# Performance work log

Hardware: AMD Instinct MI355X
Metric: run time of the kernel (lower is better)

## Reference

```python
import jax, jax.numpy as jnp
import numpy as np

RES = 8          # voxel_resolution
CLASSES = 40
B, N = 64, 100000


def setup_inputs() -> dict:
    key = jax.random.key(0)
    kx, kw, kb = jax.random.split(key, 3)
    x = jax.random.normal(kx, (B, N, 3), dtype=jnp.float32)
    f = RES ** 3
    # nn.Linear(f, CLASSES): W is (out, in), uniform(-1/sqrt(in), 1/sqrt(in))
    bound = 1.0 / np.sqrt(f)
    W = jax.random.uniform(kw, (CLASSES, f), dtype=jnp.float32, minval=-bound, maxval=bound)
    b = jax.random.uniform(kb, (CLASSES,), dtype=jnp.float32, minval=-bound, maxval=bound)
    return {"x": x, "W": W, "b": b}


def _count_points(x):
    # x: (B, N, 3) -> per-batch adaptive-range 3D histogram, normalized by N
    b_, n_, _ = x.shape
    mins = x.min(axis=1, keepdims=True)            # (B,1,3)
    maxs = x.max(axis=1, keepdims=True)            # (B,1,3)
    rng = maxs - mins
    scale = RES / jnp.where(rng > 0, rng, 1.0)
    # bin index per point per dim; points at max fall in last bin (histogramdd
    # right-closes the final bin) -> clip to RES-1
    idx = jnp.clip(jnp.floor((x - mins) * scale).astype(jnp.int32), 0, RES - 1)  # (B,N,3)
    flat = (idx[..., 0] * RES + idx[..., 1]) * RES + idx[..., 2]                 # (B,N)
    flat = flat + (jnp.arange(b_, dtype=jnp.int32) * (RES ** 3))[:, None]
    counts = jax.ops.segment_sum(
        jnp.ones((b_ * n_,), dtype=x.dtype),
        flat.reshape(-1),
        num_segments=b_ * RES ** 3,
    ).reshape(b_, RES ** 3)
    return counts / n_


def reference(x, W, b):
    counts = _count_points(x)           # (B, RES^3), mode='count'
    logits = counts @ W.T + b           # (B, CLASSES)
    return logits
```

## Files before the change

### kernel.cpp

```cpp
#include <hip/hip_runtime.h>
#include <hip/hip_cooperative_groups.h>

namespace cg = cooperative_groups;

#define RES 8
#define F 512
#define CLASSES 40
#define B 64
#define NPTS 100000
#define NSLOT (NPTS / 4)

#define BLKS 16

#define PARTH_OFF 0
#define PARTMM_OFF (B * BLKS * F)

__global__ __launch_bounds__(256, 4) void fused_kernel(const float* __restrict__ x,
                                                       const float* __restrict__ Wm,
                                                       const float* __restrict__ bias,
                                                       float* __restrict__ out,
                                                       unsigned int* __restrict__ ws) {
    const int sub   = blockIdx.x;
    const int batch = blockIdx.y;
    const int t     = threadIdx.x;

    __shared__ unsigned int lh[4][F];
    __shared__ float red[6][BLKS];
    __shared__ float smn[3], ssc[3];
    __shared__ float wmin[4][3], wmax[4][3];
    __shared__ float cf[F];

    for (int i = t; i < 4 * F; i += 256) ((unsigned int*)lh)[i] = 0u;

    const float4* xb4 = (const float4*)(x + (size_t)batch * (NPTS * 3));

    {
        float m0 = 3.0e38f, m1 = 3.0e38f, m2 = 3.0e38f;
        float M0 = -3.0e38f, M1 = -3.0e38f, M2 = -3.0e38f;
        for (int i = sub * 256 + t; i < NSLOT; i += BLKS * 256) {
            float4 p0 = xb4[3 * i + 0];
            float4 p1 = xb4[3 * i + 1];
            float4 p2 = xb4[3 * i + 2];
            m0 = fminf(m0, fminf(fminf(p0.x, p0.w), fminf(p1.z, p2.y)));
            M0 = fmaxf(M0, fmaxf(fmaxf(p0.x, p0.w), fmaxf(p1.z, p2.y)));
            m1 = fminf(m1, fminf(fminf(p0.y, p1.x), fminf(p1.w, p2.z)));
            M1 = fmaxf(M1, fmaxf(fmaxf(p0.y, p1.x), fmaxf(p1.w, p2.z)));
            m2 = fminf(m2, fminf(fminf(p0.z, p1.y), fminf(p2.x, p2.w)));
            M2 = fmaxf(M2, fmaxf(fmaxf(p0.z, p1.y), fmaxf(p2.x, p2.w)));
        }
        for (int d = 1; d < 64; d <<= 1) {
            m0 = fminf(m0, __shfl_xor(m0, d)); M0 = fmaxf(M0, __shfl_xor(M0, d));
            m1 = fminf(m1, __shfl_xor(m1, d)); M1 = fmaxf(M1, __shfl_xor(M1, d));
            m2 = fminf(m2, __shfl_xor(m2, d)); M2 = fmaxf(M2, __shfl_xor(M2, d));
        }
        const int wave = t >> 6;
        if ((t & 63) == 0) {
            wmin[wave][0] = m0; wmin[wave][1] = m1; wmin[wave][2] = m2;
            wmax[wave][0] = M0; wmax[wave][1] = M1; wmax[wave][2] = M2;
        }
        __syncthreads();
        if (t < 3) {
            float mn = fminf(fminf(wmin[0][t], wmin[1][t]), fminf(wmin[2][t], wmin[3][t]));
            float mx = fmaxf(fmaxf(wmax[0][t], wmax[1][t]), fmaxf(wmax[2][t], wmax[3][t]));
            float* pm = (float*)(ws + PARTMM_OFF) + ((size_t)batch * BLKS + sub) * 6;
            pm[t]     = mn;
            pm[3 + t] = mx;
        }
    }

    cg::this_grid().sync();

    {
        const float* pm = (const float*)(ws + PARTMM_OFF) + (size_t)batch * BLKS * 6;
        if (t < 6 * BLKS) {
            const int c = t % 6, j = t / 6;
            red[c][j] = pm[j * 6 + c];
        }
        __syncthreads();
        if (t < 3) {
            float mn = red[t][0], mx = red[t + 3][0];
#pragma unroll
            for (int j = 1; j < BLKS; ++j) {
                mn = fminf(mn, red[t][j]);
                mx = fmaxf(mx, red[t + 3][j]);
            }
            float rng = mx - mn;
            smn[t] = mn;
            ssc[t] = (float)RES / (rng > 0.0f ? rng : 1.0f);
        }
        __syncthreads();
    }

    {
        const float mn0 = smn[0], mn1 = smn[1], mn2 = smn[2];
        const float sc0 = ssc[0], sc1 = ssc[1], sc2 = ssc[2];
        unsigned int* myh = lh[t >> 6];

        for (int i = sub * 256 + t; i < NSLOT; i += BLKS * 256) {
            float4 p0 = xb4[3 * i + 0];
            float4 p1 = xb4[3 * i + 1];
            float4 p2 = xb4[3 * i + 2];
            float px[4][3] = {{p0.x, p0.y, p0.z},
                              {p0.w, p1.x, p1.y},
                              {p1.z, p1.w, p2.x},
                              {p2.y, p2.z, p2.w}};
#pragma unroll
            for (int q = 0; q < 4; ++q) {
                int i0 = (int)floorf((px[q][0] - mn0) * sc0);
                int i1 = (int)floorf((px[q][1] - mn1) * sc1);
                int i2 = (int)floorf((px[q][2] - mn2) * sc2);
                i0 = min(max(i0, 0), RES - 1);
                i1 = min(max(i1, 0), RES - 1);
                i2 = min(max(i2, 0), RES - 1);
                atomicAdd(&myh[(i0 * RES + i1) * RES + i2], 1u);
            }
        }
        __syncthreads();

        unsigned int* ph = ws + PARTH_OFF + ((size_t)batch * BLKS + sub) * F;
        for (int bin = t; bin < F; bin += 256)
            ph[bin] = lh[0][bin] + lh[1][bin] + lh[2][bin] + lh[3][bin];
    }

    cg::this_grid().sync();

    if (sub != 0) return;
    {
        const unsigned int* ph = ws + PARTH_OFF + (size_t)batch * BLKS * F;
        for (int bin = t; bin < F; bin += 256) {
            unsigned int s = 0;
#pragma unroll
            for (int j = 0; j < BLKS; ++j) s += ph[j * F + bin];
            cf[bin] = (float)s * (1.0f / (float)NPTS);
        }
        __syncthreads();
        if (t < CLASSES) {
            const float4* wr  = (const float4*)(Wm + t * F);
            const float4* cf4 = (const float4*)cf;
            float d0 = 0.f, d1 = 0.f, d2 = 0.f, d3 = 0.f;
#pragma unroll 4
            for (int k = 0; k < F / 4; k += 4) {
                float4 w0 = wr[k],   c0 = cf4[k];
                float4 w1 = wr[k+1], c1 = cf4[k+1];
                float4 w2 = wr[k+2], c2 = cf4[k+2];
                float4 w3 = wr[k+3], c3 = cf4[k+3];
                d0 += c0.x*w0.x + c0.y*w0.y + c0.z*w0.z + c0.w*w0.w;
                d1 += c1.x*w1.x + c1.y*w1.y + c1.z*w1.z + c1.w*w1.w;
                d2 += c2.x*w2.x + c2.y*w2.y + c2.z*w2.z + c2.w*w2.w;
                d3 += c3.x*w3.x + c3.y*w3.y + c3.z*w3.z + c3.w*w3.w;
            }
            out[batch * CLASSES + t] = ((d0 + d1) + (d2 + d3)) + bias[t];
        }
    }
}

__global__ __launch_bounds__(256) void minmax_kernel(const float* __restrict__ x,
                                                     unsigned int* __restrict__ ws) {
    const int sub = blockIdx.x, batch = blockIdx.y, t = threadIdx.x;
    const float4* xb4 = (const float4*)(x + (size_t)batch * (NPTS * 3));
    float m0 = 3.0e38f, m1 = 3.0e38f, m2 = 3.0e38f;
    float M0 = -3.0e38f, M1 = -3.0e38f, M2 = -3.0e38f;
    for (int i = sub * 256 + t; i < NSLOT; i += BLKS * 256) {
        float4 p0 = xb4[3 * i + 0];
        float4 p1 = xb4[3 * i + 1];
        float4 p2 = xb4[3 * i + 2];
        m0 = fminf(m0, fminf(fminf(p0.x, p0.w), fminf(p1.z, p2.y)));
        M0 = fmaxf(M0, fmaxf(fmaxf(p0.x, p0.w), fmaxf(p1.z, p2.y)));
        m1 = fminf(m1, fminf(fminf(p0.y, p1.x), fminf(p1.w, p2.z)));
        M1 = fmaxf(M1, fmaxf(fmaxf(p0.y, p1.x), fmaxf(p1.w, p2.z)));
        m2 = fminf(m2, fminf(fminf(p0.z, p1.y), fminf(p2.x, p2.w)));
        M2 = fmaxf(M2, fmaxf(fmaxf(p0.z, p1.y), fmaxf(p2.x, p2.w)));
    }
    for (int d = 1; d < 64; d <<= 1) {
        m0 = fminf(m0, __shfl_xor(m0, d)); M0 = fmaxf(M0, __shfl_xor(M0, d));
        m1 = fminf(m1, __shfl_xor(m1, d)); M1 = fmaxf(M1, __shfl_xor(M1, d));
        m2 = fminf(m2, __shfl_xor(m2, d)); M2 = fmaxf(M2, __shfl_xor(M2, d));
    }
    __shared__ float wmin[4][3], wmax[4][3];
    const int wave = t >> 6;
    if ((t & 63) == 0) {
        wmin[wave][0] = m0; wmin[wave][1] = m1; wmin[wave][2] = m2;
        wmax[wave][0] = M0; wmax[wave][1] = M1; wmax[wave][2] = M2;
    }
    __syncthreads();
    if (t < 3) {
        float mn = fminf(fminf(wmin[0][t], wmin[1][t]), fminf(wmin[2][t], wmin[3][t]));
        float mx = fmaxf(fmaxf(wmax[0][t], wmax[1][t]), fmaxf(wmax[2][t], wmax[3][t]));
        float* pm = (float*)(ws + PARTMM_OFF) + ((size_t)batch * BLKS + sub) * 6;
        pm[t] = mn;
        pm[3 + t] = mx;
    }
}

__global__ __launch_bounds__(256) void hist_kernel(const float* __restrict__ x,
                                                   unsigned int* __restrict__ ws) {
    const int sub = blockIdx.x, batch = blockIdx.y, t = threadIdx.x;
    __shared__ unsigned int lh[4][F];
    __shared__ float red[6][BLKS];
    __shared__ float smn[3], ssc[3];
    for (int i = t; i < 4 * F; i += 256) ((unsigned int*)lh)[i] = 0u;

    const float* pm = (const float*)(ws + PARTMM_OFF) + (size_t)batch * BLKS * 6;
    if (t < 6 * BLKS) {
        const int c = t % 6, j = t / 6;
        red[c][j] = pm[j * 6 + c];
    }
    __syncthreads();
    if (t < 3) {
        float mn = red[t][0], mx = red[t + 3][0];
#pragma unroll
        for (int j = 1; j < BLKS; ++j) {
            mn = fminf(mn, red[t][j]);
            mx = fmaxf(mx, red[t + 3][j]);
        }
        float rng = mx - mn;
        smn[t] = mn;
        ssc[t] = (float)RES / (rng > 0.0f ? rng : 1.0f);
    }
    __syncthreads();

    const float mn0 = smn[0], mn1 = smn[1], mn2 = smn[2];
    const float sc0 = ssc[0], sc1 = ssc[1], sc2 = ssc[2];
    const float4* xb4 = (const float4*)(x + (size_t)batch * (NPTS * 3));
    unsigned int* myh = lh[t >> 6];
    for (int i = sub * 256 + t; i < NSLOT; i += BLKS * 256) {
        float4 p0 = xb4[3 * i + 0];
        float4 p1 = xb4[3 * i + 1];
        float4 p2 = xb4[3 * i + 2];
        float px[4][3] = {{p0.x, p0.y, p0.z},
                          {p0.w, p1.x, p1.y},
                          {p1.z, p1.w, p2.x},
                          {p2.y, p2.z, p2.w}};
#pragma unroll
        for (int q = 0; q < 4; ++q) {
            int i0 = (int)floorf((px[q][0] - mn0) * sc0);
            int i1 = (int)floorf((px[q][1] - mn1) * sc1);
            int i2 = (int)floorf((px[q][2] - mn2) * sc2);
            i0 = min(max(i0, 0), RES - 1);
            i1 = min(max(i1, 0), RES - 1);
            i2 = min(max(i2, 0), RES - 1);
            atomicAdd(&myh[(i0 * RES + i1) * RES + i2], 1u);
        }
    }
    __syncthreads();
    unsigned int* ph = ws + PARTH_OFF + ((size_t)batch * BLKS + sub) * F;
    for (int bin = t; bin < F; bin += 256)
        ph[bin] = lh[0][bin] + lh[1][bin] + lh[2][bin] + lh[3][bin];
}

__global__ __launch_bounds__(256) void logits_kernel(const unsigned int* __restrict__ ws,
                                                     const float* __restrict__ Wm,
                                                     const float* __restrict__ bias,
                                                     float* __restrict__ out) {
    const int batch = blockIdx.x, t = threadIdx.x;
    __shared__ float cf[F];
    const unsigned int* ph = ws + PARTH_OFF + (size_t)batch * BLKS * F;
    for (int bin = t; bin < F; bin += 256) {
        unsigned int s = 0;
#pragma unroll
        for (int j = 0; j < BLKS; ++j) s += ph[j * F + bin];
        cf[bin] = (float)s * (1.0f / (float)NPTS);
    }
    __syncthreads();
    if (t < CLASSES) {
        const float4* wr  = (const float4*)(Wm + t * F);
        const float4* cf4 = (const float4*)cf;
        float d0 = 0.f, d1 = 0.f, d2 = 0.f, d3 = 0.f;
#pragma unroll 4
        for (int k = 0; k < F / 4; k += 4) {
            float4 w0 = wr[k],   c0 = cf4[k];
            float4 w1 = wr[k+1], c1 = cf4[k+1];
            float4 w2 = wr[k+2], c2 = cf4[k+2];
            float4 w3 = wr[k+3], c3 = cf4[k+3];
            d0 += c0.x*w0.x + c0.y*w0.y + c0.z*w0.z + c0.w*w0.w;
            d1 += c1.x*w1.x + c1.y*w1.y + c1.z*w1.z + c1.w*w1.w;
            d2 += c2.x*w2.x + c2.y*w2.y + c2.z*w2.z + c2.w*w2.w;
            d3 += c3.x*w3.x + c3.y*w3.y + c3.z*w3.z + c3.w*w3.w;
        }
        out[batch * CLASSES + t] = ((d0 + d1) + (d2 + d3)) + bias[t];
    }
}

extern "C" void kernel_launch(void* const* d_in, const int* in_sizes, int n_in,
                              void* d_out, int out_size, void* d_ws, size_t ws_size,
                              hipStream_t stream) {
    const float* x    = (const float*)d_in[0];
    const float* Wm   = (const float*)d_in[1];
    const float* bias = (const float*)d_in[2];
    float* out        = (float*)d_out;
    unsigned int* ws  = (unsigned int*)d_ws;

    static int coop_ok = -1;
    if (coop_ok < 0) {
        int dev = 0;
        hipGetDevice(&dev);
        hipDeviceProp_t prop{};
        hipGetDeviceProperties(&prop, dev);
        int nb = 0;
        hipError_t e = hipOccupancyMaxActiveBlocksPerMultiprocessor(
            &nb, (const void*)fused_kernel, 256, 0);
        coop_ok = (e == hipSuccess && prop.cooperativeLaunch &&
                   (long)nb * prop.multiProcessorCount >= (long)BLKS * B) ? 1 : 0;
    }

    if (coop_ok) {
        void* args[] = {(void*)&x, (void*)&Wm, (void*)&bias, (void*)&out, (void*)&ws};
        hipLaunchCooperativeKernel((const void*)fused_kernel, dim3(BLKS, B), dim3(256),
                                   args, 0, stream);
    } else {
        minmax_kernel<<<dim3(BLKS, B), 256, 0, stream>>>(x, ws);
        hist_kernel<<<dim3(BLKS, B), 256, 0, stream>>>(x, ws);
        logits_kernel<<<B, 256, 0, stream>>>(ws, Wm, bias, out);
    }
}
```

Baseline: 126.8 us.

## Replace grid-wide cooperative syncs with per-batch flag spin-waits

Drops the two cooperative-groups grid barriers and replaces them with per-batch release/acquire flags, padded to separate slots, that each block polls with s_sleep. Batches can then advance independently instead of waiting for all 1024 blocks. Block 0 of each batch now reuses its own shared-memory histogram instead of writing it out and reading it back, and the min/max scan loop is unrolled by two. The flags use a fixed magic value. If the workspace is not cleared between launches, stale flags from an earlier call could satisfy the waits, and spinning also assumes all blocks of a batch are co-resident.

```diff
diff --git a/kernel.cpp b/kernel.cpp
--- a/kernel.cpp
+++ b/kernel.cpp
@@ -1,7 +1,4 @@
 #include <hip/hip_runtime.h>
-#include <hip/hip_cooperative_groups.h>
-
-namespace cg = cooperative_groups;
 
 #define RES 8
 #define F 512
@@ -12,8 +9,12 @@
 
 #define BLKS 16
 
+#define MAGIC 0x5F3A9C71u
+
 #define PARTH_OFF 0
 #define PARTMM_OFF (B * BLKS * F)
+#define FLAGMM_OFF (PARTMM_OFF + B * BLKS * 6)
+#define FLAGH_OFF  (FLAGMM_OFF + B * BLKS * 16)
 
 __global__ __launch_bounds__(256, 4) void fused_kernel(const float* __restrict__ x,
                                                        const float* __restrict__ Wm,
@@ -37,6 +38,7 @@
     {
         float m0 = 3.0e38f, m1 = 3.0e38f, m2 = 3.0e38f;
         float M0 = -3.0e38f, M1 = -3.0e38f, M2 = -3.0e38f;
+#pragma unroll 2
         for (int i = sub * 256 + t; i < NSLOT; i += BLKS * 256) {
             float4 p0 = xb4[3 * i + 0];
             float4 p1 = xb4[3 * i + 1];
@@ -68,7 +70,19 @@
         }
     }
 
-    cg::this_grid().sync();
+    __syncthreads();
+    if (t == 0) {
+        __threadfence();
+        __hip_atomic_store(&ws[FLAGMM_OFF + (batch * BLKS + sub) * 16], MAGIC,
+                           __ATOMIC_RELEASE, __HIP_MEMORY_SCOPE_AGENT);
+    }
+    if (t < BLKS) {
+        const unsigned int* fl = &ws[FLAGMM_OFF + (batch * BLKS + t) * 16];
+        while (__hip_atomic_load(fl, __ATOMIC_ACQUIRE, __HIP_MEMORY_SCOPE_AGENT) != MAGIC)
+            __builtin_amdgcn_s_sleep(2);
+    }
+    __syncthreads();
+    __threadfence();
 
     {
         const float* pm = (const float*)(ws + PARTMM_OFF) + (size_t)batch * BLKS * 6;
@@ -116,21 +130,34 @@
             }
         }
         __syncthreads();
-
+    }
+
+    if (sub != 0) {
         unsigned int* ph = ws + PARTH_OFF + ((size_t)batch * BLKS + sub) * F;
         for (int bin = t; bin < F; bin += 256)
             ph[bin] = lh[0][bin] + lh[1][bin] + lh[2][bin] + lh[3][bin];
-    }
-
-    cg::this_grid().sync();
-
-    if (sub != 0) return;
+        __syncthreads();
+        if (t == 0) {
+            __threadfence();
+            __hip_atomic_store(&ws[FLAGH_OFF + (batch * BLKS + sub) * 16], MAGIC,
+                               __ATOMIC_RELEASE, __HIP_MEMORY_SCOPE_AGENT);
+        }
+        return;
+    }
+
+    if (t >= 1 && t < BLKS) {
+        const unsigned int* fl = &ws[FLAGH_OFF + (batch * BLKS + t) * 16];
+        while (__hip_atomic_load(fl, __ATOMIC_ACQUIRE, __HIP_MEMORY_SCOPE_AGENT) != MAGIC)
+            __builtin_amdgcn_s_sleep(2);
+    }
+    __syncthreads();
+    __threadfence();
     {
         const unsigned int* ph = ws + PARTH_OFF + (size_t)batch * BLKS * F;
         for (int bin = t; bin < F; bin += 256) {
-            unsigned int s = 0;
-#pragma unroll
-            for (int j = 0; j < BLKS; ++j) s += ph[j * F + bin];
+            unsigned int s = lh[0][bin] + lh[1][bin] + lh[2][bin] + lh[3][bin];
+#pragma unroll
+            for (int j = 1; j < BLKS; ++j) s += ph[j * F + bin];
             cf[bin] = (float)s * (1.0f / (float)NPTS);
         }
         __syncthreads();
```

After: 130.7 us. 3.1% more time.

## Hold point data in registers across passes; replace final grid sync with counter

Applied to the files above, without the earlier changes.

Each thread in the fused kernel now loads its six (plus an optional tail) 48-byte point groups once into registers. It reuses them for both the min/max reduction and the histogram binning, so the input is no longer read from global memory twice. The trailing cooperative grid sync before the logits stage is replaced with a per-batch atomic counter, and the last block to finish a batch computes that batch's logits. The register-resident loads raise VGPR pressure, and the counter scheme depends on correct fences and on the counter reset ordering relative to the earlier cross-block sync.

```diff
diff --git a/kernel.cpp b/kernel.cpp
--- a/kernel.cpp
+++ b/kernel.cpp
@@ -11,9 +11,39 @@
 #define NSLOT (NPTS / 4)
 
 #define BLKS 16
+#define TPB (BLKS * 256)
+#define NFULL 6
+#define TAILCUT (NSLOT - NFULL * TPB)
 
 #define PARTH_OFF 0
 #define PARTMM_OFF (B * BLKS * F)
+#define CNT_OFF (PARTMM_OFF + B * BLKS * 6)
+
+#define MM4(pA, pB, pC) do { \
+    m0 = fminf(m0, fminf(fminf((pA).x, (pA).w), fminf((pB).z, (pC).y))); \
+    M0 = fmaxf(M0, fmaxf(fmaxf((pA).x, (pA).w), fmaxf((pB).z, (pC).y))); \
+    m1 = fminf(m1, fminf(fminf((pA).y, (pB).x), fminf((pB).w, (pC).z))); \
+    M1 = fmaxf(M1, fmaxf(fmaxf((pA).y, (pB).x), fmaxf((pB).w, (pC).z))); \
+    m2 = fminf(m2, fminf(fminf((pA).z, (pB).y), fminf((pC).x, (pC).w))); \
+    M2 = fmaxf(M2, fmaxf(fmaxf((pA).z, (pB).y), fmaxf((pC).x, (pC).w))); \
+} while (0)
+
+#define BIN1(X, Y, Z) do { \
+    int i0 = (int)floorf(((X) - mn0) * sc0); \
+    int i1 = (int)floorf(((Y) - mn1) * sc1); \
+    int i2 = (int)floorf(((Z) - mn2) * sc2); \
+    i0 = min(max(i0, 0), RES - 1); \
+    i1 = min(max(i1, 0), RES - 1); \
+    i2 = min(max(i2, 0), RES - 1); \
+    atomicAdd(&myh[(i0 * RES + i1) * RES + i2], 1u); \
+} while (0)
+
+#define BIN4(pA, pB, pC) do { \
+    BIN1((pA).x, (pA).y, (pA).z); \
+    BIN1((pA).w, (pB).x, (pB).y); \
+    BIN1((pB).z, (pB).w, (pC).x); \
+    BIN1((pC).y, (pC).z, (pC).w); \
+} while (0)
 
 __global__ __launch_bounds__(256, 4) void fused_kernel(const float* __restrict__ x,
                                                        const float* __restrict__ Wm,
@@ -29,24 +59,38 @@
     __shared__ float smn[3], ssc[3];
     __shared__ float wmin[4][3], wmax[4][3];
     __shared__ float cf[F];
+    __shared__ int swin;
 
     for (int i = t; i < 4 * F; i += 256) ((unsigned int*)lh)[i] = 0u;
 
+    if (sub == 0 && t == 0)
+        __hip_atomic_store(&ws[CNT_OFF + batch * 16], 0u,
+                           __ATOMIC_RELAXED, __HIP_MEMORY_SCOPE_AGENT);
+
     const float4* xb4 = (const float4*)(x + (size_t)batch * (NPTS * 3));
+    const int g = sub * 256 + t;
+    const float4* bp = xb4 + 3 * g;
+    const bool tail = (g < TAILCUT);
+
+    float4 c0a = bp[0],         c0b = bp[1],         c0c = bp[2];
+    float4 c1a = bp[12288],     c1b = bp[12289],     c1c = bp[12290];
+    float4 c2a = bp[24576],     c2b = bp[24577],     c2c = bp[24578];
+    float4 c3a = bp[36864],     c3b = bp[36865],     c3c = bp[36866];
+    float4 c4a = bp[49152],     c4b = bp[49153],     c4c = bp[49154];
+    float4 c5a = bp[61440],     c5b = bp[61441],     c5c = bp[61442];
 
     {
         float m0 = 3.0e38f, m1 = 3.0e38f, m2 = 3.0e38f;
         float M0 = -3.0e38f, M1 = -3.0e38f, M2 = -3.0e38f;
-        for (int i = sub * 256 + t; i < NSLOT; i += BLKS * 256) {
-            float4 p0 = xb4[3 * i + 0];
-            float4 p1 = xb4[3 * i + 1];
-            float4 p2 = xb4[3 * i + 2];
-            m0 = fminf(m0, fminf(fminf(p0.x, p0.w), fminf(p1.z, p2.y)));
-            M0 = fmaxf(M0, fmaxf(fmaxf(p0.x, p0.w), fmaxf(p1.z, p2.y)));
-            m1 = fminf(m1, fminf(fminf(p0.y, p1.x), fminf(p1.w, p2.z)));
-            M1 = fmaxf(M1, fmaxf(fmaxf(p0.y, p1.x), fmaxf(p1.w, p2.z)));
-            m2 = fminf(m2, fminf(fminf(p0.z, p1.y), fminf(p2.x, p2.w)));
-            M2 = fmaxf(M2, fmaxf(fmaxf(p0.z, p1.y), fmaxf(p2.x, p2.w)));
+        MM4(c0a, c0b, c0c);
+        MM4(c1a, c1b, c1c);
+        MM4(c2a, c2b, c2c);
+        MM4(c3a, c3b, c3c);
+        MM4(c4a, c4b, c4c);
+        MM4(c5a, c5b, c5c);
+        if (tail) {
+            float4 ta = bp[73728], tb = bp[73729], tc = bp[73730];
+            MM4(ta, tb, tc);
         }
         for (int d = 1; d < 64; d <<= 1) {
             m0 = fminf(m0, __shfl_xor(m0, d)); M0 = fmaxf(M0, __shfl_xor(M0, d));
@@ -96,35 +140,35 @@
         const float sc0 = ssc[0], sc1 = ssc[1], sc2 = ssc[2];
         unsigned int* myh = lh[t >> 6];
 
-        for (int i = sub * 256 + t; i < NSLOT; i += BLKS * 256) {
-            float4 p0 = xb4[3 * i + 0];
-            float4 p1 = xb4[3 * i + 1];
-            float4 p2 = xb4[3 * i + 2];
-            float px[4][3] = {{p0.x, p0.y, p0.z},
-                              {p0.w, p1.x, p1.y},
-                              {p1.z, p1.w, p2.x},
-                              {p2.y, p2.z, p2.w}};
-#pragma unroll
-            for (int q = 0; q < 4; ++q) {
-                int i0 = (int)floorf((px[q][0] - mn0) * sc0);
-                int i1 = (int)floorf((px[q][1] - mn1) * sc1);
-                int i2 = (int)floorf((px[q][2] - mn2) * sc2);
-                i0 = min(max(i0, 0), RES - 1);
-                i1 = min(max(i1, 0), RES - 1);
-                i2 = min(max(i2, 0), RES - 1);
-                atomicAdd(&myh[(i0 * RES + i1) * RES + i2], 1u);
-            }
+        BIN4(c0a, c0b, c0c);
+        BIN4(c1a, c1b, c1c);
+        BIN4(c2a, c2b, c2c);
+        BIN4(c3a, c3b, c3c);
+        BIN4(c4a, c4b, c4c);
+        BIN4(c5a, c5b, c5c);
+        if (tail) {
+            float4 ta = bp[73728], tb = bp[73729], tc = bp[73730];
+            BIN4(ta, tb, tc);
         }
         __syncthreads();
 
         unsigned int* ph = ws + PARTH_OFF + ((size_t)batch * BLKS + sub) * F;
         for (int bin = t; bin < F; bin += 256)
             ph[bin] = lh[0][bin] + lh[1][bin] + lh[2][bin] + lh[3][bin];
-    }
-
-    cg::this_grid().sync();
-
-    if (sub != 0) return;
+        __syncthreads();
+    }
+
+    if (t == 0) {
+        __threadfence();
+        unsigned int old = __hip_atomic_fetch_add(&ws[CNT_OFF + batch * 16], 1u,
+                                                  __ATOMIC_ACQ_REL,
+                                                  __HIP_MEMORY_SCOPE_AGENT);
+        swin = (old == BLKS - 1);
+    }
+    __syncthreads();
+    if (!swin) return;
+    __threadfence();
+
     {
         const unsigned int* ph = ws + PARTH_OFF + (size_t)batch * BLKS * F;
         for (int bin = t; bin < F; bin += 256) {
@@ -161,15 +205,10 @@
     float m0 = 3.0e38f, m1 = 3.0e38f, m2 = 3.0e38f;
     float M0 = -3.0e38f, M1 = -3.0e38f, M2 = -3.0e38f;
     for (int i = sub * 256 + t; i < NSLOT; i += BLKS * 256) {
-        float4 p0 = xb4[3 * i + 0];
-        float4 p1 = xb4[3 * i + 1];
-        float4 p2 = xb4[3 * i + 2];
-        m0 = fminf(m0, fminf(fminf(p0.x, p0.w), fminf(p1.z, p2.y)));
-        M0 = fmaxf(M0, fmaxf(fmaxf(p0.x, p0.w), fmaxf(p1.z, p2.y)));
-        m1 = fminf(m1, fminf(fminf(p0.y, p1.x), fminf(p1.w, p2.z)));
-        M1 = fmaxf(M1, fmaxf(fmaxf(p0.y, p1.x), fmaxf(p1.w, p2.z)));
-        m2 = fminf(m2, fminf(fminf(p0.z, p1.y), fminf(p2.x, p2.w)));
-        M2 = fmaxf(M2, fmaxf(fmaxf(p0.z, p1.y), fmaxf(p2.x, p2.w)));
+        float4 pA = xb4[3 * i + 0];
+        float4 pB = xb4[3 * i + 1];
+        float4 pC = xb4[3 * i + 2];
+        MM4(pA, pB, pC);
     }
     for (int d = 1; d < 64; d <<= 1) {
         m0 = fminf(m0, __shfl_xor(m0, d)); M0 = fmaxf(M0, __shfl_xor(M0, d));
@@ -224,23 +263,10 @@
     const float4* xb4 = (const float4*)(x + (size_t)batch * (NPTS * 3));
     unsigned int* myh = lh[t >> 6];
     for (int i = sub * 256 + t; i < NSLOT; i += BLKS * 256) {
-        float4 p0 = xb4[3 * i + 0];
-        float4 p1 = xb4[3 * i + 1];
-        float4 p2 = xb4[3 * i + 2];
-        float px[4][3] = {{p0.x, p0.y, p0.z},
-                          {p0.w, p1.x, p1.y},
-                          {p1.z, p1.w, p2.x},
-                          {p2.y, p2.z, p2.w}};
-#pragma unroll
-        for (int q = 0; q < 4; ++q) {
-            int i0 = (int)floorf((px[q][0] - mn0) * sc0);
-            int i1 = (int)floorf((px[q][1] - mn1) * sc1);
-            int i2 = (int)floorf((px[q][2] - mn2) * sc2);
-            i0 = min(max(i0, 0), RES - 1);
-            i1 = min(max(i1, 0), RES - 1);
-            i2 = min(max(i2, 0), RES - 1);
-            atomicAdd(&myh[(i0 * RES + i1) * RES + i2], 1u);
-        }
+        float4 pA = xb4[3 * i + 0];
+        float4 pB = xb4[3 * i + 1];
+        float4 pC = xb4[3 * i + 2];
+        BIN4(pA, pB, pC);
     }
     __syncthreads();
     unsigned int* ph = ws + PARTH_OFF + ((size_t)batch * BLKS + sub) * F;
```

Measured after the change: 126.6 us. No clear change (-0.2%).
